# Performance work log

Measured on AMD Instinct MI355X. Metric: run time of the kernel, lower is better.

The kernel has to match this reference:

```python
import jax, jax.numpy as jnp
import numpy as np
from jax.scipy.special import logsumexp

DEN_SCALE = 1.0  # den_scale from LFMMILoss.__init__


def _log_marginal(em, seqlens, logA, log_start, log_final):
    """Forward (alpha) recursion of a WFSA in log space.
    em: [B,T,S] per-state emission log-likelihoods; logA: [S,S] or [B,S,S].
    Returns per-sequence log-marginal [B].
    """
    B, T, S = em.shape
    alpha0 = log_start + em[:, 0]  # [B,S]

    def step(alpha, xs):
        em_t, t = xs
        # [B,S,1] + [.,S,S] -> logsumexp over source state
        new = logsumexp(alpha[:, :, None] + logA, axis=1) + em_t
        alpha = jnp.where((t < seqlens)[:, None], new, alpha)
        return alpha, None

    em_t_first = jnp.swapaxes(em, 0, 1)  # [T,B,S]
    alpha, _ = jax.lax.scan(step, alpha0, (em_t_first[1:], jnp.arange(1, T)))
    return logsumexp(alpha + log_final, axis=1)  # [B]


def _fsm_logprob(x, seqlens, logA, log_start, log_final, pdf_ids):
    B, T, _ = x.shape
    if pdf_ids.ndim == 1:  # shared graph (denominator)
        em = x[:, :, pdf_ids]  # [B,T,S]
    else:  # per-utterance graphs (numerators), pdf_ids: [B,S]
        S = pdf_ids.shape[-1]
        idx = jnp.broadcast_to(pdf_ids[:, None, :], (B, T, S))
        em = jnp.take_along_axis(x, idx, axis=2)
    return _log_marginal(em, seqlens, logA, log_start, log_final)


def setup_inputs() -> dict:
    key = jax.random.key(0)
    ks = jax.random.split(key, 10)
    B, T, C = 16, 500, 2048
    S_num, S_den = 64, 512
    inp = jax.random.normal(ks[0], (B, T, C), jnp.float32)
    seqlengths = jax.random.randint(ks[1], (B,), T // 2, T + 1, jnp.int32)
    num_logA = jax.nn.log_softmax(jax.random.normal(ks[2], (B, S_num, S_num), jnp.float32), axis=-1)
    num_log_start = jax.nn.log_softmax(jax.random.normal(ks[3], (B, S_num), jnp.float32), axis=-1)
    num_log_final = jax.nn.log_softmax(jax.random.normal(ks[4], (B, S_num), jnp.float32), axis=-1)
    num_pdf_ids = jax.random.randint(ks[5], (B, S_num), 0, C, jnp.int32)
    den_logA = jax.nn.log_softmax(jax.random.normal(ks[6], (S_den, S_den), jnp.float32), axis=-1)
    den_log_start = jax.nn.log_softmax(jax.random.normal(ks[7], (S_den,), jnp.float32), axis=-1)
    den_log_final = jax.nn.log_softmax(jax.random.normal(ks[8], (S_den,), jnp.float32), axis=-1)
    den_pdf_ids = jax.random.randint(ks[9], (S_den,), 0, C, jnp.int32)
    return {
        "input": inp, "seqlengths": seqlengths,
        "num_logA": num_logA, "num_log_start": num_log_start,
        "num_log_final": num_log_final, "num_pdf_ids": num_pdf_ids,
        "den_logA": den_logA, "den_log_start": den_log_start,
        "den_log_final": den_log_final, "den_pdf_ids": den_pdf_ids,
    }


def reference(input, seqlengths, num_logA, num_log_start, num_log_final,
              num_pdf_ids, den_logA, den_log_start, den_log_final, den_pdf_ids):
    x = jnp.clip(input, -30.0, 30.0)
    num_llh = _fsm_logprob(x, seqlengths, num_logA, num_log_start, num_log_final, num_pdf_ids).sum()
    den_llh = _fsm_logprob(x, seqlengths, den_logA, den_log_start, den_log_final, den_pdf_ids).sum()
    return -(num_llh - DEN_SCALE * den_llh)
```

## Files before the change

### kernel.cpp

```cpp
#include <hip/hip_runtime.h>
#include <math.h>

#define BB 16
#define TT 500
#define CC 2048
#define SN 64
#define SD 512
#define NGRP 16
#define NCB 8
#define NDEN 128
#define NTHR 512
#define SHIFTC 30.0f

#define WSF_DACC   32768
#define WSF_DSCALE 32784
#define WSF_NACC   32800
#define WSF_NSCALE 32816

#define AL(p) __hip_atomic_load((p), __ATOMIC_RELAXED, __HIP_MEMORY_SCOPE_AGENT)
#define AS(p, v) __hip_atomic_store((p), (v), __ATOMIC_RELAXED, __HIP_MEMORY_SCOPE_AGENT)

typedef float f4 __attribute__((ext_vector_type(4)));

__device__ __forceinline__ float wave_max(float v) {
  #pragma unroll
  for (int off = 32; off > 0; off >>= 1) v = fmaxf(v, __shfl_xor(v, off, 64));
  return v;
}
__device__ __forceinline__ float wave_sum(float v) {
  #pragma unroll
  for (int off = 32; off > 0; off >>= 1) v += __shfl_xor(v, off, 64);
  return v;
}
__device__ __forceinline__ unsigned long long pk(unsigned tag, float v) {
  return ((unsigned long long)tag << 32) | (unsigned long long)__float_as_uint(v);
}
__device__ __forceinline__ float clamp30(float v) {
  return fminf(fmaxf(v, -30.f), 30.f);
}
__device__ __forceinline__ float rlane(float v, int k) {
  return __uint_as_float(__builtin_amdgcn_readlane(__float_as_uint(v), k));
}

__global__ __launch_bounds__(NTHR, 1) void fsm_fwd(
    const float* __restrict__ x, const int* __restrict__ seqlens,
    const float* __restrict__ nA, const float* __restrict__ nls,
    const float* __restrict__ nlf, const int* __restrict__ npdf,
    const float* __restrict__ dA, const float* __restrict__ dls,
    const float* __restrict__ dlf, const int* __restrict__ dpdf,
    unsigned long long* __restrict__ p64, float* __restrict__ wsf)
{
  __shared__ float prt[2][8 * 64];
  __shared__ float pmx[2][8];
  const int tid = threadIdx.x;
  const int lane = tid & 63, wv = tid >> 6;

  if (blockIdx.x < NDEN) {
    const int g  = blockIdx.x & 15;
    const int cb = blockIdx.x >> 4;
    const int j0 = cb * 64;

    f4 Areg[16];
    {
      const float* Ap = dA + (wv * 64) * SD + j0 + lane;
      #pragma unroll
      for (int k = 0; k < 64; ++k)
        Areg[k >> 2][k & 3] = __expf(Ap[k * SD]);
      #pragma unroll
      for (int r = 0; r < 16; ++r)
        asm volatile("" : "+v"(Areg[r]));
    }

    unsigned long long* gb0 = p64 + (size_t)g * SD;
    unsigned long long* gb1 = p64 + (size_t)(NGRP + g) * SD;

    int pdfj = 0, sl = 0; float lfj = 0.f, pcur = 0.f, scale = SHIFTC;
    if (wv == 0) {
      pdfj = dpdf[j0 + lane];
      lfj  = dlf[j0 + lane];
      sl   = seqlens[g];
      float xv = clamp30(x[g * (TT * CC) + pdfj]);
      pcur = __expf(dls[j0 + lane] + xv - SHIFTC);
      AS(gb0 + j0 + lane, pk(0u, pcur));
    }

    for (int t = 1; t < TT; ++t) {
      unsigned long long* gin  = (t & 1) ? gb0 : gb1;
      unsigned long long* gout = (t & 1) ? gb1 : gb0;
      float xv = 0.f;
      if (wv == 0)
        xv = clamp30(x[g * (TT * CC) + t * CC + pdfj]);

      const unsigned tg = (unsigned)(t - 1);
      unsigned long long* pa = gin + wv * 64 + lane;
      unsigned long long w;
      for (;;) {
        w = AL(pa);
        if ((unsigned)(w >> 32) == tg) break;
        __builtin_amdgcn_s_sleep(1);
      }
      float pv = __uint_as_float((unsigned)w);

      float cm = wave_max(pv);
      if (lane == 0) pmx[t & 1][wv] = cm;

      float q = 0.f;
      #pragma unroll
      for (int k = 0; k < 64; ++k) {
        float pk_ = rlane(pv, k);
        q = fmaf(pk_, Areg[k >> 2][k & 3], q);
      }
      prt[t & 1][wv * 64 + lane] = q;
      __syncthreads();

      if (wv == 0) {
        const float* pb = prt[t & 1];
        float qq = 0.f;
        #pragma unroll
        for (int w8 = 0; w8 < 8; ++w8) qq += pb[w8 * 64 + lane];
        float m = pmx[t & 1][0];
        #pragma unroll
        for (int w8 = 1; w8 < 8; ++w8) m = fmaxf(m, pmx[t & 1][w8]);
        float lm = __logf(m);
        if (t < sl) {
          pcur = qq * __expf(xv - SHIFTC - lm);
          scale += SHIFTC + lm;
        }
        AS(gout + j0 + lane, pk((unsigned)t, pcur));
      }
    }
    if (wv == 0) {
      float part = wave_sum(pcur * __expf(lfj));
      if (lane == 0) {
        atomicAdd(wsf + WSF_DACC + g, part);
        if (cb == 0) wsf[WSF_DSCALE + g] = scale;
      }
    }
  } else {
    const int b = blockIdx.x - NDEN;
    if (wv != 0) return;

    f4 Areg[16];
    {
      const float* Ap = nA + b * SN * SN + lane;
      #pragma unroll
      for (int i = 0; i < 64; ++i)
        Areg[i >> 2][i & 3] = __expf(Ap[i * SN]);
      #pragma unroll
      for (int r = 0; r < 16; ++r)
        asm volatile("" : "+v"(Areg[r]));
    }
    const int   pdfj = npdf[b * SN + lane];
    const float lfj  = nlf[b * SN + lane];
    const int   sl   = seqlens[b];
    float xv0 = clamp30(x[b * (TT * CC) + pdfj]);
    float pcur = __expf(nls[b * SN + lane] + xv0 - SHIFTC);
    float scale = SHIFTC;
    float xn = clamp30(x[b * (TT * CC) + CC + pdfj]);

    for (int t = 1; t < TT; ++t) {
      float xv = xn;
      if (t + 1 < TT)
        xn = clamp30(x[b * (TT * CC) + (t + 1) * CC + pdfj]);
      float pold = pcur;
      float q = 0.f;
      #pragma unroll
      for (int i = 0; i < 64; ++i) {
        float pi = rlane(pold, i);
        q = fmaf(pi, Areg[i >> 2][i & 3], q);
      }
      float lm = __logf(wave_max(pold));
      if (t < sl) {
        pcur = q * __expf(xv - SHIFTC - lm);
        scale += SHIFTC + lm;
      }
    }
    float part = wave_sum(pcur * __expf(lfj));
    if (lane == 0) {
      wsf[WSF_NACC + b]   = part;
      wsf[WSF_NSCALE + b] = scale;
    }
  }
}

__global__ void fsm_final(const float* __restrict__ wsf, float* __restrict__ out) {
  const int tid = threadIdx.x;
  float v = 0.f;
  if (tid < 16)
    v = -(wsf[WSF_NSCALE + tid] + __logf(wsf[WSF_NACC + tid]));
  else if (tid < 32)
    v = (wsf[WSF_DSCALE + tid - 16] + __logf(wsf[WSF_DACC + tid - 16]));
  v = wave_sum(v);
  if (tid == 0) out[0] = v;
}

extern "C" void kernel_launch(void* const* d_in, const int* in_sizes, int n_in,
                              void* d_out, int out_size, void* d_ws, size_t ws_size,
                              hipStream_t stream) {
  const float* x    = (const float*)d_in[0];
  const int*   sql  = (const int*)d_in[1];
  const float* nA   = (const float*)d_in[2];
  const float* nls  = (const float*)d_in[3];
  const float* nlf  = (const float*)d_in[4];
  const int*   npdf = (const int*)d_in[5];
  const float* dA   = (const float*)d_in[6];
  const float* dls  = (const float*)d_in[7];
  const float* dlf  = (const float*)d_in[8];
  const int*   dpdf = (const int*)d_in[9];
  float* out = (float*)d_out;
  unsigned long long* p64 = (unsigned long long*)d_ws;
  float* wsf = (float*)d_ws;
  (void)in_sizes; (void)n_in; (void)out_size; (void)ws_size;

  hipMemsetAsync((char*)d_ws + 131072, 0, 256, stream);
  fsm_fwd<<<NDEN + BB, NTHR, 0, stream>>>(x, sql, nA, nls, nlf, npdf,
                                          dA, dls, dlf, dpdf, p64, wsf);
  fsm_final<<<1, 64, 0, stream>>>(wsf, out);
}
```

Baseline: 890.5 us.

## Interleave two denominator sequences per workgroup to hide cross-block sync latency

Each denominator workgroup now handles two batch sequences, alternating between them each timestep, which halves the denominator workgroup count from 128 to 64. While one sequence's partial results are published, the block prefetches the other sequence's inbound records and emissions, so polling latency on the global-memory handoff overlaps with compute. This adds a second __syncthreads per step and serialises two recursions per block, which could lengthen the critical path if the overlap does not hide enough latency.

```diff
diff --git a/kernel.cpp b/kernel.cpp
--- a/kernel.cpp
+++ b/kernel.cpp
@@ -7,8 +7,7 @@
 #define SN 64
 #define SD 512
 #define NGRP 16
-#define NCB 8
-#define NDEN 128
+#define NDENWG 64
 #define NTHR 512
 #define SHIFTC 30.0f
 
@@ -40,6 +39,10 @@
 }
 __device__ __forceinline__ float rlane(float v, int k) {
   return __uint_as_float(__builtin_amdgcn_readlane(__float_as_uint(v), k));
+}
+__device__ __forceinline__ unsigned long long* recbase(
+    unsigned long long* p64, int g, int tag) {
+  return p64 + ((tag & 1) ? (size_t)(NGRP + g) : (size_t)g) * SD;
 }
 
 __global__ __launch_bounds__(NTHR, 1) void fsm_fwd(
@@ -50,15 +53,16 @@
     const float* __restrict__ dlf, const int* __restrict__ dpdf,
     unsigned long long* __restrict__ p64, float* __restrict__ wsf)
 {
-  __shared__ float prt[2][8 * 64];
-  __shared__ float pmx[2][8];
+  __shared__ float prt[2][2][8][64];
+  __shared__ float pmx[2][2][8];
   const int tid = threadIdx.x;
   const int lane = tid & 63, wv = tid >> 6;
 
-  if (blockIdx.x < NDEN) {
-    const int g  = blockIdx.x & 15;
-    const int cb = blockIdx.x >> 4;
+  if (blockIdx.x < NDENWG) {
+    const int gp = blockIdx.x & 7;
+    const int cb = blockIdx.x >> 3;
     const int j0 = cb * 64;
+    const int g0 = gp, g1 = gp + 8;
 
     f4 Areg[16];
     {
@@ -71,73 +75,116 @@
         asm volatile("" : "+v"(Areg[r]));
     }
 
-    unsigned long long* gb0 = p64 + (size_t)g * SD;
-    unsigned long long* gb1 = p64 + (size_t)(NGRP + g) * SD;
-
-    int pdfj = 0, sl = 0; float lfj = 0.f, pcur = 0.f, scale = SHIFTC;
+    int pdfj = 0, sl0 = 0, sl1 = 0;
+    float lfj = 0.f, pc0 = 0.f, pc1 = 0.f, sc0 = SHIFTC, sc1 = SHIFTC;
     if (wv == 0) {
       pdfj = dpdf[j0 + lane];
       lfj  = dlf[j0 + lane];
-      sl   = seqlens[g];
-      float xv = clamp30(x[g * (TT * CC) + pdfj]);
-      pcur = __expf(dls[j0 + lane] + xv - SHIFTC);
-      AS(gb0 + j0 + lane, pk(0u, pcur));
-    }
+      sl0  = seqlens[g0];
+      sl1  = seqlens[g1];
+      float ls = dls[j0 + lane];
+      pc0 = __expf(ls + clamp30(x[g0 * (TT * CC) + pdfj]) - SHIFTC);
+      pc1 = __expf(ls + clamp30(x[g1 * (TT * CC) + pdfj]) - SHIFTC);
+      AS(recbase(p64, g0, 0) + j0 + lane, pk(0u, pc0));
+      AS(recbase(p64, g1, 0) + j0 + lane, pk(0u, pc1));
+    }
+    unsigned long long pf = AL(recbase(p64, g0, 0) + wv * 64 + lane);
+    float xvp = 0.f, xvn = 0.f;
+    if (wv == 0) xvp = clamp30(x[g0 * (TT * CC) + CC + pdfj]);
 
     for (int t = 1; t < TT; ++t) {
-      unsigned long long* gin  = (t & 1) ? gb0 : gb1;
-      unsigned long long* gout = (t & 1) ? gb1 : gb0;
-      float xv = 0.f;
-      if (wv == 0)
-        xv = clamp30(x[g * (TT * CC) + t * CC + pdfj]);
-
       const unsigned tg = (unsigned)(t - 1);
-      unsigned long long* pa = gin + wv * 64 + lane;
-      unsigned long long w;
-      for (;;) {
-        w = AL(pa);
-        if ((unsigned)(w >> 32) == tg) break;
-        __builtin_amdgcn_s_sleep(1);
-      }
-      float pv = __uint_as_float((unsigned)w);
-
-      float cm = wave_max(pv);
-      if (lane == 0) pmx[t & 1][wv] = cm;
-
-      float q = 0.f;
-      #pragma unroll
-      for (int k = 0; k < 64; ++k) {
-        float pk_ = rlane(pv, k);
-        q = fmaf(pk_, Areg[k >> 2][k & 3], q);
-      }
-      prt[t & 1][wv * 64 + lane] = q;
-      __syncthreads();
-
-      if (wv == 0) {
-        const float* pb = prt[t & 1];
-        float qq = 0.f;
+
+      {
+        unsigned long long* pa = recbase(p64, g0, t - 1) + wv * 64 + lane;
+        unsigned long long w = pf;
+        while ((unsigned)(w >> 32) != tg) {
+          w = AL(pa);
+          if ((unsigned)(w >> 32) == tg) break;
+          __builtin_amdgcn_s_sleep(1);
+        }
+        float pv = __uint_as_float((unsigned)w);
+        float cm = wave_max(pv);
+        if (lane == 0) pmx[0][t & 1][wv] = cm;
+        float q = 0.f;
         #pragma unroll
-        for (int w8 = 0; w8 < 8; ++w8) qq += pb[w8 * 64 + lane];
-        float m = pmx[t & 1][0];
+        for (int k = 0; k < 64; ++k)
+          q = fmaf(rlane(pv, k), Areg[k >> 2][k & 3], q);
+        prt[0][t & 1][wv][lane] = q;
+        pf = AL(recbase(p64, g1, t - 1) + wv * 64 + lane);
+        if (wv == 0) xvn = clamp30(x[g1 * (TT * CC) + t * CC + pdfj]);
+        __syncthreads();
+        if (wv == 0) {
+          float qq = 0.f;
+          #pragma unroll
+          for (int w8 = 0; w8 < 8; ++w8) qq += prt[0][t & 1][w8][lane];
+          float m = pmx[0][t & 1][0];
+          #pragma unroll
+          for (int w8 = 1; w8 < 8; ++w8) m = fmaxf(m, pmx[0][t & 1][w8]);
+          float lm = __logf(m);
+          if (t < sl0) {
+            pc0 = qq * __expf(xvp - SHIFTC - lm);
+            sc0 += SHIFTC + lm;
+          }
+          AS(recbase(p64, g0, t) + j0 + lane, pk((unsigned)t, pc0));
+          xvp = xvn;
+        }
+      }
+
+      {
+        unsigned long long* pa = recbase(p64, g1, t - 1) + wv * 64 + lane;
+        unsigned long long w = pf;
+        while ((unsigned)(w >> 32) != tg) {
+          w = AL(pa);
+          if ((unsigned)(w >> 32) == tg) break;
+          __builtin_amdgcn_s_sleep(1);
+        }
+        float pv = __uint_as_float((unsigned)w);
+        float cm = wave_max(pv);
+        if (lane == 0) pmx[1][t & 1][wv] = cm;
+        float q = 0.f;
         #pragma unroll
-        for (int w8 = 1; w8 < 8; ++w8) m = fmaxf(m, pmx[t & 1][w8]);
-        float lm = __logf(m);
-        if (t < sl) {
-          pcur = qq * __expf(xv - SHIFTC - lm);
-          scale += SHIFTC + lm;
-        }
-        AS(gout + j0 + lane, pk((unsigned)t, pcur));
-      }
-    }
+        for (int k = 0; k < 64; ++k)
+          q = fmaf(rlane(pv, k), Areg[k >> 2][k & 3], q);
+        prt[1][t & 1][wv][lane] = q;
+        if (t + 1 < TT) {
+          pf = AL(recbase(p64, g0, t) + wv * 64 + lane);
+          if (wv == 0) xvn = clamp30(x[g0 * (TT * CC) + (t + 1) * CC + pdfj]);
+        }
+        __syncthreads();
+        if (wv == 0) {
+          float qq = 0.f;
+          #pragma unroll
+          for (int w8 = 0; w8 < 8; ++w8) qq += prt[1][t & 1][w8][lane];
+          float m = pmx[1][t & 1][0];
+          #pragma unroll
+          for (int w8 = 1; w8 < 8; ++w8) m = fmaxf(m, pmx[1][t & 1][w8]);
+          float lm = __logf(m);
+          if (t < sl1) {
+            pc1 = qq * __expf(xvp - SHIFTC - lm);
+            sc1 += SHIFTC + lm;
+          }
+          AS(recbase(p64, g1, t) + j0 + lane, pk((unsigned)t, pc1));
+          xvp = xvn;
+        }
+      }
+    }
+
     if (wv == 0) {
-      float part = wave_sum(pcur * __expf(lfj));
+      float e = __expf(lfj);
+      float part0 = wave_sum(pc0 * e);
+      float part1 = wave_sum(pc1 * e);
       if (lane == 0) {
-        atomicAdd(wsf + WSF_DACC + g, part);
-        if (cb == 0) wsf[WSF_DSCALE + g] = scale;
+        atomicAdd(wsf + WSF_DACC + g0, part0);
+        atomicAdd(wsf + WSF_DACC + g1, part1);
+        if (cb == 0) {
+          wsf[WSF_DSCALE + g0] = sc0;
+          wsf[WSF_DSCALE + g1] = sc1;
+        }
       }
     }
   } else {
-    const int b = blockIdx.x - NDEN;
+    const int b = blockIdx.x - NDENWG;
     if (wv != 0) return;
 
     f4 Areg[16];
@@ -213,7 +260,7 @@
   (void)in_sizes; (void)n_in; (void)out_size; (void)ws_size;
 
   hipMemsetAsync((char*)d_ws + 131072, 0, 256, stream);
-  fsm_fwd<<<NDEN + BB, NTHR, 0, stream>>>(x, sql, nA, nls, nlf, npdf,
-                                          dA, dls, dlf, dpdf, p64, wsf);
+  fsm_fwd<<<NDENWG + BB, NTHR, 0, stream>>>(x, sql, nA, nls, nlf, npdf,
+                                            dA, dls, dlf, dpdf, p64, wsf);
   fsm_final<<<1, 64, 0, stream>>>(wsf, out);
 }
```

Result: slower. 1.530 ms (+71.8%).
